# Performance work log

Hardware: AMD Instinct MI355X
Metric: run time of the kernel (lower is better)

The kernel has to match this reference:

```python
import math
import jax, jax.numpy as jnp
import numpy as np

D_MODEL = 1024
N_HEAD = 16
HEAD_DIM = D_MODEL // N_HEAD
MAX_LENGTH = 2048


def sinusoid_table():
    # Matches RelativeEmbedding.get_embedding with num_embeddings = max_length + 1
    num_emb = MAX_LENGTH + 1
    half = HEAD_DIM // 2
    freq = jnp.exp(jnp.arange(half, dtype=jnp.float32) * (-math.log(10000.0) / (half - 1)))
    lo = -((num_emb + 1) // 2)  # python floor of -num_emb//2
    hi = num_emb // 2
    pos = jnp.arange(lo, hi, dtype=jnp.float32)  # length num_emb
    ang = pos[:, None] * freq[None, :]
    table = jnp.concatenate([jnp.sin(ang), jnp.cos(ang)], axis=1)  # (num_emb, HEAD_DIM)
    origin_shift = num_emb // 2 + 1
    return table, origin_shift


def _shift(BD):
    # (b, n, L, 2L) -> (b, n, L, L) diagonal-shift trick
    b, n, L, _ = BD.shape
    BD = jnp.concatenate([BD, jnp.zeros((b, n, L, 1), BD.dtype)], axis=-1)
    BD = BD.reshape(b, n, -1, L)[:, :, :-1, :].reshape(b, n, L, -1)
    return BD[:, :, :, :L]


def setup_inputs() -> dict:
    key = jax.random.key(0)
    k1, k2, k3, k4 = jax.random.split(key, 4)
    B, L = 2, 1024
    x = jax.random.normal(k1, (B, L, D_MODEL), dtype=jnp.float32)
    mask = jnp.ones((B, L), dtype=jnp.int32)
    W_qv = jax.random.normal(k2, (2 * D_MODEL, D_MODEL), dtype=jnp.float32) * 0.02
    r_r_bias = jax.random.normal(k3, (N_HEAD, HEAD_DIM), dtype=jnp.float32) * 0.02
    r_w_bias = jax.random.normal(k4, (N_HEAD, HEAD_DIM), dtype=jnp.float32) * 0.02
    return {"x": x, "mask": mask, "W_qv": W_qv, "r_r_bias": r_r_bias, "r_w_bias": r_w_bias}


def reference(x, mask, W_qv, r_r_bias, r_w_bias):
    B, L, d = x.shape
    table, origin_shift = sinusoid_table()
    pos = jnp.arange(-L, L) + origin_shift
    pos_embed = table[pos]  # (2L, head_dim)

    qv = x @ W_qv.T  # (B, L, 2d)
    q, v = jnp.split(qv, 2, axis=-1)
    q = q.reshape(B, L, N_HEAD, HEAD_DIM).transpose(0, 2, 1, 3)  # (B,H,L,dh)
    k = x.reshape(B, L, N_HEAD, HEAD_DIM).transpose(0, 2, 1, 3)
    v = v.reshape(B, L, N_HEAD, HEAD_DIM).transpose(0, 2, 1, 3)

    AC = jnp.einsum('bnqd,bnkd->bnqk', q + r_r_bias[None, :, None, :], k)
    D_ = jnp.einsum('nd,ld->nl', r_w_bias, pos_embed)[None, :, None, :]  # (1,H,1,2L)
    B_ = jnp.einsum('bnqd,ld->bnql', q, pos_embed)  # (B,H,L,2L)
    BD = _shift(B_ + D_)

    attn = AC + BD
    attn = jnp.where(mask[:, None, None, :] == 0, -jnp.inf, attn)
    attn = jax.nn.softmax(attn, axis=-1)
    out = jnp.einsum('bnqk,bnkd->bnqd', attn, v)
    return out.transpose(0, 2, 1, 3).reshape(B, L, d)
```

## Files before the change

### kernel.cpp

```cpp
#include <hip/hip_runtime.h>
#include <hip/hip_bf16.h>
#include <math.h>

#define L_SEQ 1024
#define TWO_L 2048
#define NHEAD 16
#define HD 64
#define DM 1024
#define BATCH 2
#define PE2R 2176
#define GBS 132

typedef _Float16 f16;
typedef _Float16 f16x4 __attribute__((ext_vector_type(4)));
typedef _Float16 f16x8 __attribute__((ext_vector_type(8)));
typedef float f32x4 __attribute__((ext_vector_type(4)));

__device__ __forceinline__ f16x8 ld8(const f16* p) {
  f16x4 lo = *(const f16x4*)p;
  f16x4 hi = *(const f16x4*)(p + 16);
  f16x8 r;
  r[0] = lo[0]; r[1] = lo[1]; r[2] = lo[2]; r[3] = lo[3];
  r[4] = hi[0]; r[5] = hi[1]; r[6] = hi[2]; r[7] = hi[3];
  return r;
}

__device__ __forceinline__ float pe_val(int j, int d) {
  float posval = (float)(j - L_SEQ);
  float freq = expf(-(float)(d & 31) * 0.2971077539347156f);
  float ang = posval * freq;
  return (d < 32) ? sinf(ang) : cosf(ang);
}

__global__ __launch_bounds__(256) void prep1(const float* __restrict__ x,
                                             const float* __restrict__ W,
                                             f16* __restrict__ pe2,
                                             f16* __restrict__ xh,
                                             f16* __restrict__ Wh) {
  int bid = blockIdx.x, tid = threadIdx.x;
  if (bid < 2048) {
    int i = (bid * 256 + tid) * 4;
    float4 v = *(const float4*)(x + i);
    f16x4 o = {(f16)v.x, (f16)v.y, (f16)v.z, (f16)v.w};
    *(f16x4*)(xh + i) = o;
  } else if (bid < 4096) {
    int i = ((bid - 2048) * 256 + tid) * 4;
    float4 v = *(const float4*)(W + i);
    f16x4 o = {(f16)v.x, (f16)v.y, (f16)v.z, (f16)v.w};
    *(f16x4*)(Wh + i) = o;
  } else {
    int idx = (bid - 4096) * 256 + tid;
    int rrow = idx >> 6, d = idx & 63;
    int u = rrow - 1088;
    int j = (u < 0) ? u + 2049 : u;
    float v = (j != 2048) ? pe_val(j, d) : 0.f;
    pe2[idx] = (f16)v;
  }
}

#define QV_STEP(T, AS, BS, CA0, CA1, CB0, CB1, NA0, NA1, NB0, NB1)             \
  {                                                                            \
    *(f16x8*)&AS[r * 72 + c] = CA0;                                            \
    *(f16x8*)&AS[r * 72 + c + 8] = CA1;                                        \
    *(f16x8*)&BS[r * 72 + c] = CB0;                                            \
    *(f16x8*)&BS[r * 72 + c + 8] = CB1;                                        \
    __syncthreads();                                                           \
    if ((T) + 1 < 16) {                                                        \
      const f16* na = ga + ((T) + 1) * 64;                                     \
      NA0 = *(const f16x8*)na;                                                 \
      NA1 = *(const f16x8*)(na + 8);                                           \
      const f16* nb = gb + ((T) + 1) * 64;                                     \
      NB0 = *(const f16x8*)nb;                                                 \
      NB1 = *(const f16x8*)(nb + 8);                                           \
    }                                                                          \
    _Pragma("unroll")                                                          \
    for (int kc = 0; kc < 2; ++kc) {                                           \
      f16x8 a = ld8(&AS[(w * 16 + li) * 72 + kc * 32 + g * 4]);                \
      _Pragma("unroll")                                                        \
      for (int nf = 0; nf < 4; ++nf) {                                         \
        f16x8 bfr = ld8(&BS[(nf * 16 + li) * 72 + kc * 32 + g * 4]);           \
        s[nf] = __builtin_amdgcn_mfma_f32_16x16x32_f16(a, bfr, s[nf], 0, 0, 0);\
      }                                                                        \
    }                                                                          \
  }

__global__ __launch_bounds__(256) void qv_mfma(const f16* __restrict__ xh,
                                               const f16* __restrict__ Wh,
                                               f16* __restrict__ qvh,
                                               f16* __restrict__ vT) {
  __shared__ f16 As0[64 * 72], As1[64 * 72];
  __shared__ f16 Bs0[64 * 72], Bs1[64 * 72];
  int tid = threadIdx.x;
  int w = tid >> 6, lane = tid & 63, g = lane >> 4, li = lane & 15;
  int m0 = blockIdx.y * 64, n0 = blockIdx.x * 64;
  int r = tid >> 2, c = (tid & 3) * 16;

  const f16* ga = xh + (size_t)(m0 + r) * 1024 + c;
  const f16* gb = Wh + (size_t)(n0 + r) * 1024 + c;
  f16x8 ca0 = *(const f16x8*)ga, ca1 = *(const f16x8*)(ga + 8);
  f16x8 cb0 = *(const f16x8*)gb, cb1 = *(const f16x8*)(gb + 8);
  f16x8 na0, na1, nb0, nb1;

  f32x4 s[4];
#pragma unroll
  for (int i = 0; i < 4; ++i) s[i] = {0.f, 0.f, 0.f, 0.f};

  for (int t = 0; t < 16; t += 2) {
    QV_STEP(t, As0, Bs0, ca0, ca1, cb0, cb1, na0, na1, nb0, nb1);
    QV_STEP(t + 1, As1, Bs1, na0, na1, nb0, nb1, ca0, ca1, cb0, cb1);
  }

#pragma unroll
  for (int nf = 0; nf < 4; ++nf) {
    int n = n0 + nf * 16 + li;
#pragma unroll
    for (int rr2 = 0; rr2 < 4; ++rr2) {
      int m = m0 + w * 16 + g * 4 + rr2;
      f16 val = (f16)s[nf][rr2];
      if (n < 1024) {
        qvh[(size_t)m * 2048 + n] = val;
      } else {
        int b_ = m >> 10, ls = m & 1023, hd = n - 1024;
        vT[((size_t)(b_ * 16 + (hd >> 6)) * 64 + (hd & 63)) * 1024 + ls] = val;
      }
    }
  }
}

#define BANDFILL(TT, QOFF, PEREG)                                              \
  {                                                                            \
    _Pragma("unroll")                                                          \
    for (int qf = 0; qf < 4; ++qf) {                                           \
      f32x4 gacc = {0.f, 0.f, 0.f, 0.f};                                       \
      _Pragma("unroll")                                                        \
      for (int kc = 0; kc < 2; ++kc) {                                         \
        f16x8 qo = ld8(&Qw[((QOFF) + qf * 16 + li) * 72 + kc * 32 + g * 4]);   \
        gacc = __builtin_amdgcn_mfma_f32_16x16x32_f16(PEREG[kc], qo, gacc, 0, 0, 0); \
      }                                                                        \
      f16x4 gpk;                                                               \
      gpk[0] = (f16)gacc[0]; gpk[1] = (f16)gacc[1];                            \
      gpk[2] = (f16)gacc[2]; gpk[3] = (f16)gacc[3];                            \
      *(f16x4*)&Gb[(qf * 16 + li) * GBS + (TT) + w * 16 + g * 4] = gpk;        \
    }                                                                          \
  }

#define ATTN_STEP(T, KS, VS, CK0, CK1, CV0, CV1, NK0, NK1, NV0, NV1, CPE, NPE) \
  {                                                                            \
    const int k0 = (T) * 64;                                                   \
    const int tt = (64 * (T)) & 127;                                           \
    const int qoff = (64 * (T) >= q0) ? 1 : 0;                                 \
    *(f16x8*)&KS[r * 72 + c] = CK0;                                            \
    *(f16x8*)&KS[r * 72 + c + 8] = CK1;                                        \
    *(f16x8*)&VS[r * 72 + c] = CV0;                                            \
    *(f16x8*)&VS[r * 72 + c + 8] = CV1;                                        \
    BANDFILL(tt, qoff, CPE)                                                    \
    __syncthreads();                                                           \
    if ((T) + 1 < 16) {                                                        \
      const f16* nk = gk + (size_t)((T) + 1) * 64 * 1024;                      \
      NK0 = *(const f16x8*)nk;                                                 \
      NK1 = *(const f16x8*)(nk + 8);                                           \
      const f16* nv = gv + ((T) + 1) * 64;                                     \
      NV0 = *(const f16x8*)nv;                                                 \
      NV1 = *(const f16x8*)(nv + 8);                                           \
      const f16* pb = pe2 + (size_t)(1088 + 64 * ((T) + 1) - q0 + w * 16 + li) * 64; \
      NPE[0] = ld8(pb + g * 4);                                                \
      NPE[1] = ld8(pb + 32 + g * 4);                                           \
    }                                                                          \
    float gf[16];                                                              \
    {                                                                          \
      const int cb0 = tt + g * 4 - qi + 128;                                   \
      _Pragma("unroll")                                                        \
      for (int kf = 0; kf < 4; ++kf)                                           \
        _Pragma("unroll")                                                      \
        for (int u2 = 0; u2 < 4; ++u2)                                         \
          gf[kf * 4 + u2] = (float)Gb[qi * GBS + ((cb0 + kf * 16 + u2) & 127)];\
    }                                                                          \
    f32x4 s[4];                                                                \
    _Pragma("unroll")                                                          \
    for (int i = 0; i < 4; ++i) s[i] = {0.f, 0.f, 0.f, 0.f};                   \
    __builtin_amdgcn_s_setprio(1);                                             \
    _Pragma("unroll")                                                          \
    for (int kc = 0; kc < 2; ++kc) {                                           \
      f16x8 qb = ld8(&Qs[(1 + w * 16 + li) * 72 + kc * 32 + g * 4]);           \
      _Pragma("unroll")                                                        \
      for (int kf = 0; kf < 4; ++kf) {                                         \
        f16x8 ka = ld8(&KS[(kf * 16 + li) * 72 + kc * 32 + g * 4]);            \
        s[kf] = __builtin_amdgcn_mfma_f32_16x16x32_f16(ka, qb, s[kf], 0, 0, 0);\
      }                                                                        \
    }                                                                          \
    __builtin_amdgcn_s_setprio(0);                                             \
    float sv[16];                                                              \
    float tmax = -1e30f;                                                       \
    _Pragma("unroll")                                                          \
    for (int kf = 0; kf < 4; ++kf) {                                           \
      _Pragma("unroll")                                                        \
      for (int rr2 = 0; rr2 < 4; ++rr2) {                                      \
        float v_ = s[kf][rr2] + gf[kf * 4 + rr2] +                             \
                   Ms[k0 + kf * 16 + g * 4 + rr2];                             \
        sv[kf * 4 + rr2] = v_;                                                 \
        tmax = fmaxf(tmax, v_);                                                \
      }                                                                        \
    }                                                                          \
    tmax = fmaxf(tmax, __shfl_xor(tmax, 16));                                  \
    tmax = fmaxf(tmax, __shfl_xor(tmax, 32));                                  \
    if (!__all(tmax <= m_run + 8.f)) {                                         \
      float mnew = fmaxf(m_run, tmax);                                         \
      float scale = __expf(m_run - mnew);                                      \
      m_run = mnew;                                                            \
      l_run *= scale;                                                          \
      _Pragma("unroll")                                                        \
      for (int f = 0; f < 4; ++f) {                                            \
        o[f][0] *= scale; o[f][1] *= scale; o[f][2] *= scale; o[f][3] *= scale;\
      }                                                                        \
    }                                                                          \
    float pf[16];                                                              \
    float lloc = 0.f;                                                          \
    _Pragma("unroll")                                                          \
    for (int i = 0; i < 16; ++i) { pf[i] = __expf(sv[i] - m_run); lloc += pf[i]; } \
    l_run += lloc;                                                             \
    f16x8 pb0, pb1;                                                            \
    _Pragma("unroll")                                                          \
    for (int i = 0; i < 8; ++i) { pb0[i] = (f16)pf[i]; pb1[i] = (f16)pf[8 + i]; } \
    __builtin_amdgcn_s_setprio(1);                                             \
    _Pragma("unroll")                                                          \
    for (int f = 0; f < 4; ++f) {                                              \
      f16x8 va0 = ld8(&VS[(f * 16 + li) * 72 + g * 4]);                        \
      o[f] = __builtin_amdgcn_mfma_f32_16x16x32_f16(va0, pb0, o[f], 0, 0, 0);  \
      f16x8 va1 = ld8(&VS[(f * 16 + li) * 72 + 32 + g * 4]);                   \
      o[f] = __builtin_amdgcn_mfma_f32_16x16x32_f16(va1, pb1, o[f], 0, 0, 0);  \
    }                                                                          \
    __builtin_amdgcn_s_setprio(0);                                             \
    __syncthreads();                                                           \
  }

__global__ __launch_bounds__(256) void attn_mfma(const f16* __restrict__ xh,
                                                 const f16* __restrict__ qvh,
                                                 const f16* __restrict__ vT,
                                                 const f16* __restrict__ pe2,
                                                 const int* __restrict__ mask,
                                                 const float* __restrict__ rr,
                                                 const float* __restrict__ rw,
                                                 float* __restrict__ out) {
  __shared__ f16 Qs[65 * 72];
  __shared__ f16 Qw[65 * 72];
  __shared__ f16 Ks0[64 * 72], Ks1[64 * 72];
  __shared__ f16 Vs0[64 * 72], Vs1[64 * 72];
  __shared__ f16 Gb[64 * GBS];
  __shared__ float Ms[L_SEQ];
  int tid = threadIdx.x;
  int w = tid >> 6, lane = tid & 63, g = lane >> 4, li = lane & 15;
  int bid = blockIdx.x;
  int swz = (bid & 7) * 64 + (bid >> 3);
  int q0 = (swz & 15) * 64;
  int bh = swz >> 4;
  int b = bh >> 4, h = bh & 15;
  int r = tid >> 2, c = (tid & 3) * 16;
  const int qi = w * 16 + li;

#pragma unroll
  for (int i = 0; i < 4; ++i) {
    int k = tid + i * 256;
    Ms[k] = mask[b * L_SEQ + k] ? 0.f : -1e30f;
  }
  {
    int gq = q0 - 1 + r;
    if (gq < 0) gq = 0;
    const f16* src = qvh + (size_t)(b * L_SEQ + gq) * 2048 + h * HD + c;
#pragma unroll
    for (int u = 0; u < 16; ++u) {
      float v = (float)src[u];
      Qs[r * 72 + c + u] = (f16)(v + rr[h * HD + c + u]);
      Qw[r * 72 + c + u] = (f16)(v + rw[h * HD + c + u]);
    }
    if (tid < 4) {
      int c2 = tid * 16;
      const f16* s2 = qvh + (size_t)(b * L_SEQ + q0 + 63) * 2048 + h * HD + c2;
#pragma unroll
      for (int u = 0; u < 16; ++u) {
        float v = (float)s2[u];
        Qs[64 * 72 + c2 + u] = (f16)(v + rr[h * HD + c2 + u]);
        Qw[64 * 72 + c2 + u] = (f16)(v + rw[h * HD + c2 + u]);
      }
    }
  }

  const f16* gk = xh + (size_t)(b * L_SEQ + r) * 1024 + h * HD + c;
  const f16* gv = vT + ((size_t)bh * 64 + r) * 1024 + c;
  f16x8 cka = *(const f16x8*)gk, ckb = *(const f16x8*)(gk + 8);
  f16x8 cva = *(const f16x8*)gv, cvb = *(const f16x8*)(gv + 8);
  f16x8 nka, nkb, nva, nvb;
  f16x8 peP[2], peA[2], peB[2];
  {
    const f16* pp = pe2 + (size_t)(1024 - q0 + w * 16 + li) * 64;
    peP[0] = ld8(pp + g * 4);
    peP[1] = ld8(pp + 32 + g * 4);
    const f16* p0 = pe2 + (size_t)(1088 - q0 + w * 16 + li) * 64;
    peA[0] = ld8(p0 + g * 4);
    peA[1] = ld8(p0 + 32 + g * 4);
  }

  __syncthreads();

  BANDFILL(64, 0, peP)

  float m_run = -1e30f, l_run = 0.f;
  f32x4 o[4];
#pragma unroll
  for (int i = 0; i < 4; ++i) o[i] = {0.f, 0.f, 0.f, 0.f};

  for (int t = 0; t < 16; t += 2) {
    ATTN_STEP(t, Ks0, Vs0, cka, ckb, cva, cvb, nka, nkb, nva, nvb, peA, peB);
    ATTN_STEP(t + 1, Ks1, Vs1, nka, nkb, nva, nvb, cka, ckb, cva, cvb, peB, peA);
  }

  float lt = l_run;
  lt += __shfl_xor(lt, 16);
  lt += __shfl_xor(lt, 32);
  float inv = 1.0f / lt;
  int qrow = q0 + qi;
  float* op = out + ((size_t)(b * L_SEQ + qrow)) * DM + h * HD;
#pragma unroll
  for (int f = 0; f < 4; ++f) {
    float4 res = {o[f][0] * inv, o[f][1] * inv, o[f][2] * inv, o[f][3] * inv};
    *(float4*)(op + f * 16 + g * 4) = res;
  }
}

extern "C" void kernel_launch(void* const* d_in, const int* in_sizes, int n_in,
                              void* d_out, int out_size, void* d_ws, size_t ws_size,
                              hipStream_t stream) {
  const float* x = (const float*)d_in[0];
  const int* mask = (const int*)d_in[1];
  const float* W = (const float*)d_in[2];
  const float* rr = (const float*)d_in[3];
  const float* rw = (const float*)d_in[4];
  float* out = (float*)d_out;

  f16* pe2 = (f16*)d_ws;
  f16* xh = pe2 + (size_t)PE2R * 64;
  f16* Wh = xh + 2097152;
  f16* qvh = Wh + 2097152;
  f16* vT = qvh + 4194304;

  prep1<<<4096 + (PE2R * 64) / 256, 256, 0, stream>>>(x, W, pe2, xh, Wh);
  qv_mfma<<<dim3(32, 32), 256, 0, stream>>>(xh, Wh, qvh, vT);
  attn_mfma<<<512, 256, 0, stream>>>(xh, qvh, vT, pe2, mask, rr, rw, out);
}
```

Baseline: 85.67 us.

## Precompute per-head positional bias, fold log2e into Q, use exp2 softmax

The separate Qw tile (q + r_w_bias) is removed. The positional term is rewritten as (q + r_r_bias)·pe plus a per-head bias table (rw - rr)·pe, which a new prep1 block range precomputes. The log2(e) factor is folded into Q and the bias so the softmax can use exp2f, and the rescale threshold is adjusted to match. The mask loads are vectorised to float4. This cuts shared memory and the Q setup work, but adds a global float4 bias load per step and a serial 64-term loop in prep.

```diff
diff --git a/kernel.cpp b/kernel.cpp
--- a/kernel.cpp
+++ b/kernel.cpp
@@ -10,6 +10,7 @@
 #define BATCH 2
 #define PE2R 2176
 #define GBS 132
+#define LOG2E 1.4426950408889634f
 
 typedef _Float16 f16;
 typedef _Float16 f16x4 __attribute__((ext_vector_type(4)));
@@ -36,7 +37,10 @@
                                              const float* __restrict__ W,
                                              f16* __restrict__ pe2,
                                              f16* __restrict__ xh,
-                                             f16* __restrict__ Wh) {
+                                             f16* __restrict__ Wh,
+                                             const float* __restrict__ rr,
+                                             const float* __restrict__ rw,
+                                             float* __restrict__ D2x) {
   int bid = blockIdx.x, tid = threadIdx.x;
   if (bid < 2048) {
     int i = (bid * 256 + tid) * 4;
@@ -48,13 +52,25 @@
     float4 v = *(const float4*)(W + i);
     f16x4 o = {(f16)v.x, (f16)v.y, (f16)v.z, (f16)v.w};
     *(f16x4*)(Wh + i) = o;
-  } else {
+  } else if (bid < 4640) {
     int idx = (bid - 4096) * 256 + tid;
     int rrow = idx >> 6, d = idx & 63;
     int u = rrow - 1088;
     int j = (u < 0) ? u + 2049 : u;
     float v = (j != 2048) ? pe_val(j, d) : 0.f;
     pe2[idx] = (f16)v;
+  } else {
+    int idx = (bid - 4640) * 256 + tid;
+    int h = idx / PE2R, r0 = idx - h * PE2R;
+    int u = r0 - 1088;
+    int j = (u < 0) ? u + 2049 : u;
+    float s = 0.f;
+    if (j != 2048) {
+#pragma unroll
+      for (int d = 0; d < HD; ++d)
+        s = fmaf(rw[h * HD + d] - rr[h * HD + d], pe_val(j, d), s);
+    }
+    D2x[idx] = s * LOG2E;
   }
 }
 
@@ -127,19 +143,19 @@
   }
 }
 
-#define BANDFILL(TT, QOFF, PEREG)                                              \
+#define BANDFILL(TT, QOFF, PEREG, D2V)                                         \
   {                                                                            \
     _Pragma("unroll")                                                          \
     for (int qf = 0; qf < 4; ++qf) {                                           \
       f32x4 gacc = {0.f, 0.f, 0.f, 0.f};                                       \
       _Pragma("unroll")                                                        \
       for (int kc = 0; kc < 2; ++kc) {                                         \
-        f16x8 qo = ld8(&Qw[((QOFF) + qf * 16 + li) * 72 + kc * 32 + g * 4]);   \
+        f16x8 qo = ld8(&Qs[((QOFF) + qf * 16 + li) * 72 + kc * 32 + g * 4]);   \
         gacc = __builtin_amdgcn_mfma_f32_16x16x32_f16(PEREG[kc], qo, gacc, 0, 0, 0); \
       }                                                                        \
       f16x4 gpk;                                                               \
-      gpk[0] = (f16)gacc[0]; gpk[1] = (f16)gacc[1];                            \
-      gpk[2] = (f16)gacc[2]; gpk[3] = (f16)gacc[3];                            \
+      gpk[0] = (f16)(gacc[0] + (D2V).x); gpk[1] = (f16)(gacc[1] + (D2V).y);    \
+      gpk[2] = (f16)(gacc[2] + (D2V).z); gpk[3] = (f16)(gacc[3] + (D2V).w);    \
       *(f16x4*)&Gb[(qf * 16 + li) * GBS + (TT) + w * 16 + g * 4] = gpk;        \
     }                                                                          \
   }
@@ -153,7 +169,8 @@
     *(f16x8*)&KS[r * 72 + c + 8] = CK1;                                        \
     *(f16x8*)&VS[r * 72 + c] = CV0;                                            \
     *(f16x8*)&VS[r * 72 + c + 8] = CV1;                                        \
-    BANDFILL(tt, qoff, CPE)                                                    \
+    float4 d2v = *(const float4*)(D2x + hD2 + 1088 + k0 - q0 + w * 16 + g * 4);\
+    BANDFILL(tt, qoff, CPE, d2v)                                               \
     __syncthreads();                                                           \
     if ((T) + 1 < 16) {                                                        \
       const f16* nk = gk + (size_t)((T) + 1) * 64 * 1024;                      \
@@ -193,19 +210,20 @@
     float tmax = -1e30f;                                                       \
     _Pragma("unroll")                                                          \
     for (int kf = 0; kf < 4; ++kf) {                                           \
+      float4 ms4 = *(const float4*)&Ms[k0 + kf * 16 + g * 4];                  \
+      float msa[4] = {ms4.x, ms4.y, ms4.z, ms4.w};                             \
       _Pragma("unroll")                                                        \
       for (int rr2 = 0; rr2 < 4; ++rr2) {                                      \
-        float v_ = s[kf][rr2] + gf[kf * 4 + rr2] +                             \
-                   Ms[k0 + kf * 16 + g * 4 + rr2];                             \
+        float v_ = s[kf][rr2] + gf[kf * 4 + rr2] + msa[rr2];                   \
         sv[kf * 4 + rr2] = v_;                                                 \
         tmax = fmaxf(tmax, v_);                                                \
       }                                                                        \
     }                                                                          \
     tmax = fmaxf(tmax, __shfl_xor(tmax, 16));                                  \
     tmax = fmaxf(tmax, __shfl_xor(tmax, 32));                                  \
-    if (!__all(tmax <= m_run + 8.f)) {                                         \
+    if (!__all(tmax <= m_run + 11.544f)) {                                     \
       float mnew = fmaxf(m_run, tmax);                                         \
-      float scale = __expf(m_run - mnew);                                      \
+      float scale = exp2f(m_run - mnew);                                       \
       m_run = mnew;                                                            \
       l_run *= scale;                                                          \
       _Pragma("unroll")                                                        \
@@ -216,7 +234,7 @@
     float pf[16];                                                              \
     float lloc = 0.f;                                                          \
     _Pragma("unroll")                                                          \
-    for (int i = 0; i < 16; ++i) { pf[i] = __expf(sv[i] - m_run); lloc += pf[i]; } \
+    for (int i = 0; i < 16; ++i) { pf[i] = exp2f(sv[i] - m_run); lloc += pf[i]; } \
     l_run += lloc;                                                             \
     f16x8 pb0, pb1;                                                            \
     _Pragma("unroll")                                                          \
@@ -237,12 +255,11 @@
                                                  const f16* __restrict__ qvh,
                                                  const f16* __restrict__ vT,
                                                  const f16* __restrict__ pe2,
+                                                 const float* __restrict__ D2x,
                                                  const int* __restrict__ mask,
                                                  const float* __restrict__ rr,
-                                                 const float* __restrict__ rw,
                                                  float* __restrict__ out) {
   __shared__ f16 Qs[65 * 72];
-  __shared__ f16 Qw[65 * 72];
   __shared__ f16 Ks0[64 * 72], Ks1[64 * 72];
   __shared__ f16 Vs0[64 * 72], Vs1[64 * 72];
   __shared__ f16 Gb[64 * GBS];
@@ -256,6 +273,7 @@
   int b = bh >> 4, h = bh & 15;
   int r = tid >> 2, c = (tid & 3) * 16;
   const int qi = w * 16 + li;
+  const int hD2 = h * PE2R;
 
 #pragma unroll
   for (int i = 0; i < 4; ++i) {
@@ -267,20 +285,14 @@
     if (gq < 0) gq = 0;
     const f16* src = qvh + (size_t)(b * L_SEQ + gq) * 2048 + h * HD + c;
 #pragma unroll
-    for (int u = 0; u < 16; ++u) {
-      float v = (float)src[u];
-      Qs[r * 72 + c + u] = (f16)(v + rr[h * HD + c + u]);
-      Qw[r * 72 + c + u] = (f16)(v + rw[h * HD + c + u]);
-    }
+    for (int u = 0; u < 16; ++u)
+      Qs[r * 72 + c + u] = (f16)(((float)src[u] + rr[h * HD + c + u]) * LOG2E);
     if (tid < 4) {
       int c2 = tid * 16;
       const f16* s2 = qvh + (size_t)(b * L_SEQ + q0 + 63) * 2048 + h * HD + c2;
 #pragma unroll
-      for (int u = 0; u < 16; ++u) {
-        float v = (float)s2[u];
-        Qs[64 * 72 + c2 + u] = (f16)(v + rr[h * HD + c2 + u]);
-        Qw[64 * 72 + c2 + u] = (f16)(v + rw[h * HD + c2 + u]);
-      }
+      for (int u = 0; u < 16; ++u)
+        Qs[64 * 72 + c2 + u] = (f16)(((float)s2[u] + rr[h * HD + c2 + u]) * LOG2E);
     }
   }
 
@@ -301,7 +313,10 @@
 
   __syncthreads();
 
-  BANDFILL(64, 0, peP)
+  {
+    float4 d2p = *(const float4*)(D2x + hD2 + 1024 - q0 + w * 16 + g * 4);
+    BANDFILL(64, 0, peP, d2p)
+  }
 
   float m_run = -1e30f, l_run = 0.f;
   f32x4 o[4];
@@ -337,12 +352,13 @@
   float* out = (float*)d_out;
 
   f16* pe2 = (f16*)d_ws;
-  f16* xh = pe2 + (size_t)PE2R * 64;
+  float* D2x = (float*)(pe2 + (size_t)PE2R * 64);
+  f16* xh = (f16*)(D2x + 16 * PE2R);
   f16* Wh = xh + 2097152;
   f16* qvh = Wh + 2097152;
   f16* vT = qvh + 4194304;
 
-  prep1<<<4096 + (PE2R * 64) / 256, 256, 0, stream>>>(x, W, pe2, xh, Wh);
+  prep1<<<4640 + (16 * PE2R) / 256, 256, 0, stream>>>(x, W, pe2, xh, Wh, rr, rw, D2x);
   qv_mfma<<<dim3(32, 32), 256, 0, stream>>>(xh, Wh, qvh, vT);
-  attn_mfma<<<512, 256, 0, stream>>>(xh, qvh, vT, pe2, mask, rr, rw, out);
-}
+  attn_mfma<<<512, 256, 0, stream>>>(xh, qvh, vT, pe2, D2x, mask, rr, out);
+}
```

After: 103.8 us. 21.1% more time.
